# Kernel tuning notes

Hardware: AMD Instinct MI355X
Metric: run time of the kernel (lower is better)

The kernel has to match this reference:

```python
import jax, jax.numpy as jnp
import numpy as np
from jax import lax

DN2 = ('NCHW', 'OIHW', 'NCHW')
DN3 = ('NCDHW', 'OIDHW', 'NCDHW')


def _convlstm_step(h, c, x, W, b):
    # x: [B, Cin, H, W], h/c: [B, nf, H, W], W: [4*nf, Cin+nf, 3, 3]
    comb = jnp.concatenate([x, h], axis=1)
    cc = lax.conv_general_dilated(comb, W, (1, 1), 'SAME', dimension_numbers=DN2)
    cc = cc + b[None, :, None, None]
    ci, cf, co, cg = jnp.split(cc, 4, axis=1)
    i = jax.nn.sigmoid(ci)
    f = jax.nn.sigmoid(cf)
    o = jax.nn.sigmoid(co)
    g = jnp.tanh(cg)
    c_next = f * c + i * g
    h_next = o * jnp.tanh(c_next)
    return h_next, c_next


def setup_inputs() -> dict:
    key = jax.random.key(0)
    ks = jax.random.split(key, 4)
    B, T, Cin, H, W = 32, 12, 1, 64, 64
    nf = 64
    s = 0.05
    return {
        'x': jax.random.normal(ks[0], (B, T, Cin, H, W), jnp.float32),
        'future_step': 12,
        'W_enc': jax.random.normal(ks[1], (4 * nf, Cin + nf, 3, 3), jnp.float32) * s,
        'b_enc': jnp.zeros((4 * nf,), jnp.float32),
        'W_dec': jax.random.normal(ks[2], (4 * nf, nf + nf, 3, 3), jnp.float32) * s,
        'b_dec': jnp.zeros((4 * nf,), jnp.float32),
        'W_cnn': jax.random.normal(ks[3], (1, nf, 1, 3, 3), jnp.float32) * s,
        'b_cnn': jnp.zeros((1,), jnp.float32),
    }


def reference(x, future_step, W_enc, b_enc, W_dec, b_dec, W_cnn, b_cnn):
    B, T, Cin, H, Wd = x.shape
    nf = W_enc.shape[0] // 4
    h0 = jnp.zeros((B, nf, H, Wd), x.dtype)
    c0 = jnp.zeros((B, nf, H, Wd), x.dtype)

    # ---- encoder: scan over time ----
    def enc_step(carry, xt):
        h, c = carry
        h, c = _convlstm_step(h, c, xt, W_enc, b_enc)
        return (h, c), None

    (h_t, _), _ = lax.scan(enc_step, (h0, c0), jnp.moveaxis(x, 1, 0))
    encoder_vector = h_t
    out_encoder_vector = encoder_vector.reshape(B, -1)

    # ---- decoder: feed back h as next input ----
    def dec_step(carry, _):
        ev, h, c = carry
        h, c = _convlstm_step(h, c, ev, W_dec, b_dec)
        return (h, h, c), h

    _, outs = lax.scan(dec_step, (encoder_vector, h0, c0), None, length=future_step)
    # outs: [Tf, B, nf, H, W] -> [B, nf, Tf, H, W]
    outs = jnp.transpose(outs, (1, 2, 0, 3, 4))

    # ---- 3D CNN head: kernel (1,3,3), padding (0,1,1) ----
    y = lax.conv_general_dilated(outs, W_cnn, (1, 1, 1),
                                 [(0, 0), (1, 1), (1, 1)],
                                 dimension_numbers=DN3)
    y = y + b_cnn[None, :, None, None, None]
    # [B, 1, Tf, H, W] -> [B, Tf, 1, H, W]
    y = jnp.transpose(y, (0, 2, 1, 3, 4))
    return y, out_encoder_vector
```

## Files before the change

kernel.cpp:

```cpp
#include <hip/hip_runtime.h>
#include <hip/hip_bf16.h>


#define HW 4096
#define NF 64

typedef __attribute__((ext_vector_type(8))) short bf16x8;
typedef __attribute__((ext_vector_type(4))) float f32x4;

__device__ __forceinline__ float fsig(float v) {
  return __builtin_amdgcn_rcpf(1.f + __expf(-v));
}
__device__ __forceinline__ float ftanh(float v) {
  float vc = fminf(fmaxf(v, -15.f), 15.f);
  float e = __expf(2.f * vc);
  return (e - 1.f) * __builtin_amdgcn_rcpf(e + 1.f);
}
__device__ __forceinline__ float bf2f(short s) {
  union { unsigned u; float f; } a;
  a.u = ((unsigned)(unsigned short)s) << 16;
  return a.f;
}
__device__ __forceinline__ short f2bf(float f) {
  union { float f; unsigned u; } a;
  a.f = f;
  unsigned r = (a.u + 0x7fff + ((a.u >> 16) & 1)) >> 16;
  return (short)r;
}

template <bool HAS_X>
__global__ __launch_bounds__(512) void lstm_mfma_k(
    const short* __restrict__ hin,
    const short* __restrict__ W,
    const float* __restrict__ wx,
    const float* __restrict__ xpl,
    const float* __restrict__ bias,
    const float* __restrict__ cin,
    short* __restrict__ hout,
    float* __restrict__ cout) {
  const int y0 = blockIdx.x * 2;
  const int b = blockIdx.y;
  const int tid = threadIdx.x;
  const int lane = tid & 63;
  const int wv = tid >> 6;
  const int wnf = wv & 3;
  const int wrow = wv >> 2;
  const int col = lane & 15;
  const int quad = lane >> 4;

  __shared__ short As[2][16384];
  __shared__ short Bs[4 * 66 * 64];
  __shared__ float xs[4][64];

  const short* hb = hin + (size_t)b * (HW * 64);
#pragma unroll
  for (int i = 0; i < 4; ++i) {
    const int t = tid + i * 512;
    const int r = t >> 9;
    const int c = t & 511;
    const int px = c >> 3, ch0 = (c & 7) * 8;
    const int py = y0 - 1 + r;
    bf16x8 v = {0, 0, 0, 0, 0, 0, 0, 0};
    if (py >= 0 && py < 64)
      v = *reinterpret_cast<const bf16x8*>(hb + ((py * 64 + px) * 64) + ch0);
    *reinterpret_cast<bf16x8*>(
        &Bs[(((r * 66 + px + 1) * 64) + ch0) ^ ((((px + 1) & 7)) << 3)]) = v;
  }
  if (tid < 64) {
    const int r = tid >> 4;
    const int s = ((tid >> 3) & 1) * 65;
    const int ch0 = (tid & 7) * 8;
    bf16x8 z = {0, 0, 0, 0, 0, 0, 0, 0};
    *reinterpret_cast<bf16x8*>(
        &Bs[(((r * 66 + s) * 64) + ch0) ^ ((s & 7) << 3)]) = z;
  }
#pragma unroll
  for (int i = 0; i < 4; ++i) {
    const int q = tid + i * 512;
    *reinterpret_cast<bf16x8*>(&As[0][q * 8]) =
        *reinterpret_cast<const bf16x8*>(W + q * 8);
  }
  if (HAS_X) {
    if (tid < 256) {
      const float* xb = xpl + (size_t)b * (12 * HW);
      const int r = tid >> 6, cx = tid & 63;
      const int py = y0 - 1 + r;
      xs[r][cx] = (py >= 0 && py < 64) ? xb[py * 64 + cx] : 0.f;
    }
  }
  __syncthreads();

  f32x4 acc[4][4];
#pragma unroll
  for (int g = 0; g < 4; ++g) {
    const int oc0 = g * 64 + wnf * 16 + quad * 4;
#pragma unroll
    for (int nt = 0; nt < 4; ++nt)
#pragma unroll
      for (int r = 0; r < 4; ++r) acc[g][nt][r] = bias[oc0 + r];
  }

  if (HAS_X) {
#pragma unroll
    for (int nt = 0; nt < 4; ++nt) {
      const int px = nt * 16 + col;
#pragma unroll
      for (int tap = 0; tap < 9; ++tap) {
        const int pxx = px + (tap % 3) - 1;
        const float xv =
            (pxx >= 0 && pxx < 64) ? xs[wrow + tap / 3][pxx] : 0.f;
#pragma unroll
        for (int g = 0; g < 4; ++g) {
          const int oc0 = g * 64 + wnf * 16 + quad * 4;
#pragma unroll
          for (int r = 0; r < 4; ++r)
            acc[g][nt][r] = fmaf(xv, wx[(oc0 + r) * 9 + tap], acc[g][nt][r]);
        }
      }
    }
  }

  const int axr = (col & 7) << 3;
#pragma unroll
  for (int tap = 0; tap < 9; ++tap) {
    bf16x8 anx[4];
    if (tap < 8) {
#pragma unroll
      for (int i = 0; i < 4; ++i) {
        const int q = tid + i * 512;
        anx[i] = *reinterpret_cast<const bf16x8*>(W + (tap + 1) * 16384 + q * 8);
      }
    }
    const int hr = wrow + tap / 3;
    const int sb = col + (tap % 3);
    const int sx = (sb & 7) << 3;
#pragma unroll
    for (int kc = 0; kc < 2; ++kc) {
      const int chb = kc * 32 + quad * 8;
      const int abase = (((wnf * 16 + col) * 64) + chb) ^ axr;
      const int bbase = (((hr * 66 + sb) * 64) + chb) ^ sx;
      bf16x8 a[4], bfr[4];
#pragma unroll
      for (int g = 0; g < 4; ++g)
        a[g] = *reinterpret_cast<const bf16x8*>(&As[tap & 1][abase + g * 4096]);
#pragma unroll
      for (int nt = 0; nt < 4; ++nt)
        bfr[nt] = *reinterpret_cast<const bf16x8*>(&Bs[bbase + nt * 1024]);
#pragma unroll
      for (int g = 0; g < 4; ++g)
#pragma unroll
        for (int nt = 0; nt < 4; ++nt)
          acc[g][nt] = __builtin_amdgcn_mfma_f32_16x16x32_bf16(a[g], bfr[nt],
                                                               acc[g][nt], 0, 0, 0);
    }
    if (tap < 8) {
#pragma unroll
      for (int i = 0; i < 4; ++i) {
        const int q = tid + i * 512;
        *reinterpret_cast<bf16x8*>(&As[(tap & 1) ^ 1][q * 8]) = anx[i];
      }
      __syncthreads();
    }
  }

  const int nf0 = wnf * 16 + quad * 4;
  const int y = y0 + wrow;
#pragma unroll
  for (int nt = 0; nt < 4; ++nt) {
    const int px = nt * 16 + col;
    const size_t pix = (size_t)b * HW + y * 64 + px;
    f32x4 cold = *reinterpret_cast<const f32x4*>(cin + pix * 64 + nf0);
    f32x4 cnew;
    short hnew[4];
#pragma unroll
    for (int r = 0; r < 4; ++r) {
      float i_ = fsig(acc[0][nt][r]);
      float f_ = fsig(acc[1][nt][r]);
      float o_ = fsig(acc[2][nt][r]);
      float g_ = ftanh(acc[3][nt][r]);
      float cn = fmaf(f_, cold[r], i_ * g_);
      cnew[r] = cn;
      hnew[r] = f2bf(o_ * ftanh(cn));
    }
    *reinterpret_cast<f32x4*>(cout + pix * 64 + nf0) = cnew;
    short4 hv = make_short4(hnew[0], hnew[1], hnew[2], hnew[3]);
    *reinterpret_cast<short4*>(hout + pix * 64 + nf0) = hv;
  }
}

__global__ __launch_bounds__(256) void head_k(const short* __restrict__ h,
                                              const float* __restrict__ wc2,
                                              const float* __restrict__ bc,
                                              float* __restrict__ yout, int t) {
  const int tid = blockIdx.x * 256 + threadIdx.x;
  const int pix = tid & 4095;
  const int b = tid >> 12;
  const int x0 = pix & 63, y0 = pix >> 6;
  float acc = bc[0];
  const short* hb = h + (size_t)b * (HW * 64);
#pragma unroll
  for (int tap = 0; tap < 9; ++tap) {
    const int yy = y0 + tap / 3 - 1, xx = x0 + (tap % 3) - 1;
    if (yy < 0 || yy > 63 || xx < 0 || xx > 63) continue;
    const short* hp = hb + (yy * 64 + xx) * 64;
    const float* wp = wc2 + tap * 64;
#pragma unroll
    for (int f8 = 0; f8 < 8; ++f8) {
      bf16x8 v = *reinterpret_cast<const bf16x8*>(hp + f8 * 8);
#pragma unroll
      for (int j = 0; j < 8; ++j) acc = fmaf(wp[f8 * 8 + j], bf2f(v[j]), acc);
    }
  }
  yout[(size_t)(b * 12 + t) * HW + pix] = acc;
}

__global__ __launch_bounds__(256) void ev_out_k(const short* __restrict__ h,
                                                float* __restrict__ out) {
  __shared__ float tl[64][65];
  const int b = blockIdx.y, pg = blockIdx.x;
  const int p0 = pg * 64;
  {
    const int pixl = threadIdx.x >> 2, c0 = (threadIdx.x & 3) * 16;
    const short* hp = h + ((size_t)b * HW + p0 + pixl) * 64 + c0;
#pragma unroll
    for (int i = 0; i < 16; ++i) tl[pixl][c0 + i] = bf2f(hp[i]);
  }
  __syncthreads();
  {
    const int ch = threadIdx.x >> 2, q0 = (threadIdx.x & 3) * 16;
    float* op = out + ((size_t)b * 64 + ch) * (size_t)HW + p0 + q0;
#pragma unroll
    for (int i = 0; i < 16; ++i) op[i] = tl[q0 + i][ch];
  }
}

__global__ __launch_bounds__(256) void reo_enc_k(const float* __restrict__ src,
                                                 short* __restrict__ Wh,
                                                 float* __restrict__ wx) {
  const int idx = blockIdx.x * 256 + threadIdx.x;
  if (idx < 9 * 256 * 64) {
    const int tap = idx >> 14, oc = (idx >> 6) & 255, c = idx & 63;
    const int dst = tap * 16384 + (((oc * 64) + c) ^ ((oc & 7) << 3));
    Wh[dst] = f2bf(src[(oc * 65 + (c + 1)) * 9 + tap]);
  }
  if (idx < 256 * 9) {
    const int oc = idx / 9, tap = idx % 9;
    wx[idx] = src[(oc * 65 + 0) * 9 + tap];
  }
}

__global__ __launch_bounds__(256) void reo_dec_k(const float* __restrict__ src,
                                                 short* __restrict__ Wx,
                                                 short* __restrict__ Ws) {
  const int idx = blockIdx.x * 256 + threadIdx.x;
  if (idx >= 9 * 256 * 64) return;
  const int tap = idx >> 14, oc = (idx >> 6) & 255, c = idx & 63;
  const int dst = tap * 16384 + (((oc * 64) + c) ^ ((oc & 7) << 3));
  const float a = src[(oc * 128 + c) * 9 + tap];
  const float b = src[(oc * 128 + 64 + c) * 9 + tap];
  Wx[dst] = f2bf(a);
  Ws[dst] = f2bf(a + b);
}

__global__ __launch_bounds__(256) void reo_cnn_k(const float* __restrict__ src,
                                                 float* __restrict__ wc2) {
  const int idx = blockIdx.x * 256 + threadIdx.x;
  if (idx >= 576) return;
  wc2[idx] = src[(idx % 64) * 9 + (idx / 64)];
}

extern "C" void kernel_launch(void* const* d_in, const int* in_sizes, int n_in,
                              void* d_out, int out_size, void* d_ws, size_t ws_size,
                              hipStream_t stream) {
  const float* x = (const float*)d_in[0];
  const float* W_enc = (const float*)d_in[2];
  const float* b_enc = (const float*)d_in[3];
  const float* W_dec = (const float*)d_in[4];
  const float* b_dec = (const float*)d_in[5];
  const float* W_cnn = (const float*)d_in[6];
  const float* b_cnn = (const float*)d_in[7];
  float* out = (float*)d_out;
  float* out_y = out;
  float* out_ev = out + 1572864;

  float* ws = (float*)d_ws;
  float* cA = ws;
  float* cB = cA + 8388608;
  short* hA = (short*)(cB + 8388608);
  short* hB = hA + 8388608;
  short* WEh = hB + 8388608;
  short* WDx = WEh + 147456;
  short* WDs = WDx + 147456;
  float* wx = (float*)(WDs + 147456);
  float* wc2 = wx + 2304;

  reo_enc_k<<<(147456 + 255) / 256, 256, 0, stream>>>(W_enc, WEh, wx);
  reo_dec_k<<<(147456 + 255) / 256, 256, 0, stream>>>(W_dec, WDx, WDs);
  reo_cnn_k<<<3, 256, 0, stream>>>(W_cnn, wc2);

  hipMemsetAsync(hA, 0, 8388608 * sizeof(short), stream);
  hipMemsetAsync(cA, 0, 8388608 * sizeof(float), stream);

  dim3 gridL(32, 32), blkL(512);
  dim3 gridE(64, 32), blkE(256);
  short *ha = hA, *hb = hB;
  float *ca = cA, *cb = cB;

  for (int t = 0; t < 12; ++t) {
    lstm_mfma_k<true><<<gridL, blkL, 0, stream>>>(ha, WEh, wx, x + t * HW,
                                                  b_enc, ca, hb, cb);
    { short* tm = ha; ha = hb; hb = tm; }
    { float* tm = ca; ca = cb; cb = tm; }
  }
  ev_out_k<<<gridE, blkE, 0, stream>>>(ha, out_ev);

  hipMemsetAsync(cb, 0, 8388608 * sizeof(float), stream);
  { float* tm = ca; ca = cb; cb = tm; }

  for (int t = 0; t < 12; ++t) {
    lstm_mfma_k<false><<<gridL, blkL, 0, stream>>>(
        ha, (t == 0) ? WDx : WDs, nullptr, nullptr, b_dec, ca, hb, cb);
    { short* tm = ha; ha = hb; hb = tm; }
    { float* tm = ca; ca = cb; cb = tm; }
    head_k<<<512, 256, 0, stream>>>(ha, wc2, b_cnn, out_y, t);
  }
}
```

Before: 2.200 ms.

## Load LSTM conv weights directly into registers and shrink blocks to one row

The ConvLSTM kernel no longer stages the per-tap weight slab in shared memory with a barrier per tap. Each wave now reads its A fragments straight from global memory, prefetched one K-chunk ahead, and the weight reorder kernels drop the swizzle. Blocks shrink to 256 threads covering one image row, with the grid swapped to (batch, row), smaller shared memory and launch bounds asking for 4 blocks per CU, plus s_setprio around the MFMA loop. This removes the LDS traffic and syncs for weights, at the cost of more redundant global or L2 weight reads and more halo loads per output row.

Result: slower. 4.322 ms (+96.4%).

```diff
diff --git a/kernel.cpp b/kernel.cpp
--- a/kernel.cpp
+++ b/kernel.cpp
@@ -29,7 +29,7 @@
 }
 
 template <bool HAS_X>
-__global__ __launch_bounds__(512) void lstm_mfma_k(
+__global__ __launch_bounds__(256, 4) void lstm_mfma_k(
     const short* __restrict__ hin,
     const short* __restrict__ W,
     const float* __restrict__ wx,
@@ -38,35 +38,32 @@
     const float* __restrict__ cin,
     short* __restrict__ hout,
     float* __restrict__ cout) {
-  const int y0 = blockIdx.x * 2;
-  const int b = blockIdx.y;
+  const int b = blockIdx.x;
+  const int y = blockIdx.y;
   const int tid = threadIdx.x;
   const int lane = tid & 63;
-  const int wv = tid >> 6;
-  const int wnf = wv & 3;
-  const int wrow = wv >> 2;
+  const int wnf = tid >> 6;
   const int col = lane & 15;
   const int quad = lane >> 4;
 
-  __shared__ short As[2][16384];
-  __shared__ short Bs[4 * 66 * 64];
-  __shared__ float xs[4][64];
+  __shared__ short Bs[3 * 66 * 64];
+  __shared__ float xs[3][64];
 
   const short* hb = hin + (size_t)b * (HW * 64);
 #pragma unroll
-  for (int i = 0; i < 4; ++i) {
-    const int t = tid + i * 512;
+  for (int i = 0; i < 6; ++i) {
+    const int t = tid + i * 256;
     const int r = t >> 9;
     const int c = t & 511;
     const int px = c >> 3, ch0 = (c & 7) * 8;
-    const int py = y0 - 1 + r;
+    const int py = y - 1 + r;
     bf16x8 v = {0, 0, 0, 0, 0, 0, 0, 0};
     if (py >= 0 && py < 64)
       v = *reinterpret_cast<const bf16x8*>(hb + ((py * 64 + px) * 64) + ch0);
     *reinterpret_cast<bf16x8*>(
         &Bs[(((r * 66 + px + 1) * 64) + ch0) ^ ((((px + 1) & 7)) << 3)]) = v;
   }
-  if (tid < 64) {
+  if (tid < 48) {
     const int r = tid >> 4;
     const int s = ((tid >> 3) & 1) * 65;
     const int ch0 = (tid & 7) * 8;
@@ -74,20 +71,21 @@
     *reinterpret_cast<bf16x8*>(
         &Bs[(((r * 66 + s) * 64) + ch0) ^ ((s & 7) << 3)]) = z;
   }
-#pragma unroll
-  for (int i = 0; i < 4; ++i) {
-    const int q = tid + i * 512;
-    *reinterpret_cast<bf16x8*>(&As[0][q * 8]) =
-        *reinterpret_cast<const bf16x8*>(W + q * 8);
-  }
   if (HAS_X) {
-    if (tid < 256) {
+    if (tid < 192) {
       const float* xb = xpl + (size_t)b * (12 * HW);
       const int r = tid >> 6, cx = tid & 63;
-      const int py = y0 - 1 + r;
+      const int py = y - 1 + r;
       xs[r][cx] = (py >= 0 && py < 64) ? xb[py * 64 + cx] : 0.f;
     }
   }
+
+  const short* Wl = W + ((wnf * 16 + col) * 64 + quad * 8);
+  bf16x8 acur[4];
+#pragma unroll
+  for (int g = 0; g < 4; ++g)
+    acur[g] = *reinterpret_cast<const bf16x8*>(Wl + g * 4096);
+
   __syncthreads();
 
   f32x4 acc[4][4];
@@ -107,8 +105,7 @@
 #pragma unroll
       for (int tap = 0; tap < 9; ++tap) {
         const int pxx = px + (tap % 3) - 1;
-        const float xv =
-            (pxx >= 0 && pxx < 64) ? xs[wrow + tap / 3][pxx] : 0.f;
+        const float xv = (pxx >= 0 && pxx < 64) ? xs[tap / 3][pxx] : 0.f;
 #pragma unroll
         for (int g = 0; g < 4; ++g) {
           const int oc0 = g * 64 + wnf * 16 + quad * 4;
@@ -120,51 +117,44 @@
     }
   }
 
-  const int axr = (col & 7) << 3;
 #pragma unroll
   for (int tap = 0; tap < 9; ++tap) {
-    bf16x8 anx[4];
-    if (tap < 8) {
-#pragma unroll
-      for (int i = 0; i < 4; ++i) {
-        const int q = tid + i * 512;
-        anx[i] = *reinterpret_cast<const bf16x8*>(W + (tap + 1) * 16384 + q * 8);
+    const int hr = tap / 3;
+    const int sb = col + tap % 3;
+    const int sx = (sb & 7) << 3;
+    const int brow = (hr * 66 + sb) * 64;
+#pragma unroll
+    for (int kc = 0; kc < 2; ++kc) {
+      bf16x8 anx[4];
+      if (!(tap == 8 && kc == 1)) {
+        const int ntap = kc ? tap + 1 : tap;
+        const int nkc = kc ^ 1;
+#pragma unroll
+        for (int g = 0; g < 4; ++g)
+          anx[g] = *reinterpret_cast<const bf16x8*>(Wl + ntap * 16384 +
+                                                    nkc * 32 + g * 4096);
       }
-    }
-    const int hr = wrow + tap / 3;
-    const int sb = col + (tap % 3);
-    const int sx = (sb & 7) << 3;
-#pragma unroll
-    for (int kc = 0; kc < 2; ++kc) {
-      const int chb = kc * 32 + quad * 8;
-      const int abase = (((wnf * 16 + col) * 64) + chb) ^ axr;
-      const int bbase = (((hr * 66 + sb) * 64) + chb) ^ sx;
-      bf16x8 a[4], bfr[4];
+      const int bb = (brow + kc * 32 + quad * 8) ^ sx;
+      bf16x8 bfr[4];
+#pragma unroll
+      for (int nt = 0; nt < 4; ++nt)
+        bfr[nt] = *reinterpret_cast<const bf16x8*>(&Bs[bb + nt * 1024]);
+      __builtin_amdgcn_s_setprio(1);
 #pragma unroll
       for (int g = 0; g < 4; ++g)
-        a[g] = *reinterpret_cast<const bf16x8*>(&As[tap & 1][abase + g * 4096]);
-#pragma unroll
-      for (int nt = 0; nt < 4; ++nt)
-        bfr[nt] = *reinterpret_cast<const bf16x8*>(&Bs[bbase + nt * 1024]);
-#pragma unroll
-      for (int g = 0; g < 4; ++g)
 #pragma unroll
         for (int nt = 0; nt < 4; ++nt)
-          acc[g][nt] = __builtin_amdgcn_mfma_f32_16x16x32_bf16(a[g], bfr[nt],
-                                                               acc[g][nt], 0, 0, 0);
-    }
-    if (tap < 8) {
-#pragma unroll
-      for (int i = 0; i < 4; ++i) {
-        const int q = tid + i * 512;
-        *reinterpret_cast<bf16x8*>(&As[(tap & 1) ^ 1][q * 8]) = anx[i];
+          acc[g][nt] = __builtin_amdgcn_mfma_f32_16x16x32_bf16(
+              acur[g], bfr[nt], acc[g][nt], 0, 0, 0);
+      __builtin_amdgcn_s_setprio(0);
+      if (!(tap == 8 && kc == 1)) {
+#pragma unroll
+        for (int g = 0; g < 4; ++g) acur[g] = anx[g];
       }
-      __syncthreads();
     }
   }
 
   const int nf0 = wnf * 16 + quad * 4;
-  const int y = y0 + wrow;
 #pragma unroll
   for (int nt = 0; nt < 4; ++nt) {
     const int px = nt * 16 + col;
@@ -240,8 +230,7 @@
   const int idx = blockIdx.x * 256 + threadIdx.x;
   if (idx < 9 * 256 * 64) {
     const int tap = idx >> 14, oc = (idx >> 6) & 255, c = idx & 63;
-    const int dst = tap * 16384 + (((oc * 64) + c) ^ ((oc & 7) << 3));
-    Wh[dst] = f2bf(src[(oc * 65 + (c + 1)) * 9 + tap]);
+    Wh[idx] = f2bf(src[(oc * 65 + (c + 1)) * 9 + tap]);
   }
   if (idx < 256 * 9) {
     const int oc = idx / 9, tap = idx % 9;
@@ -255,11 +244,10 @@
   const int idx = blockIdx.x * 256 + threadIdx.x;
   if (idx >= 9 * 256 * 64) return;
   const int tap = idx >> 14, oc = (idx >> 6) & 255, c = idx & 63;
-  const int dst = tap * 16384 + (((oc * 64) + c) ^ ((oc & 7) << 3));
   const float a = src[(oc * 128 + c) * 9 + tap];
   const float b = src[(oc * 128 + 64 + c) * 9 + tap];
-  Wx[dst] = f2bf(a);
-  Ws[dst] = f2bf(a + b);
+  Wx[idx] = f2bf(a);
+  Ws[idx] = f2bf(a + b);
 }
 
 __global__ __launch_bounds__(256) void reo_cnn_k(const float* __restrict__ src,
@@ -301,7 +289,7 @@
   hipMemsetAsync(hA, 0, 8388608 * sizeof(short), stream);
   hipMemsetAsync(cA, 0, 8388608 * sizeof(float), stream);
 
-  dim3 gridL(32, 32), blkL(512);
+  dim3 gridL(32, 64), blkL(256);
   dim3 gridE(64, 32), blkE(256);
   short *ha = hA, *hb = hB;
   float *ca = cA, *cb = cB;
```
